# Kernel optimization log

Hardware: AMD Instinct MI355X
Metric: run time of the kernel (lower is better)

Reference implementation:

```python
import jax, jax.numpy as jnp
import numpy as np

B, T, A = 512, 64, 32
E = D = H = 512
S = 32; C = 32; SD = S * C  # stoch_dim = 1024
UNIMIX = 0.01


def _ln(x, g, b):
    m = x.mean(-1, keepdims=True)
    v = x.var(-1, keepdims=True)
    return (x - m) / jnp.sqrt(v + 1e-5) * g + b


def _mish(x):
    return x * jnp.tanh(jax.nn.softplus(x))


def _unimix_logits(raw):
    # reshape [..., S*C] -> [..., S, C], mix with uniform, back to log-space
    l = raw.reshape(raw.shape[:-1] + (S, C))
    p = jax.nn.softmax(l, axis=-1)
    p = (1.0 - UNIMIX) * p + UNIMIX / C
    return jnp.log(jnp.clip(p, 1e-8))


def setup_inputs() -> dict:
    key = jax.random.key(0)
    ks = jax.random.split(key, 16)
    n = lambda k, shape, s=0.02: (jax.random.normal(k, shape) * s).astype(jnp.float32)
    return {
        "actions": jax.random.normal(ks[0], (B, T, A), jnp.float32),
        "embeds": jax.random.normal(ks[1], (B, T, E), jnp.float32),
        # action_proj: Linear(A,H) + LayerNorm(H)
        "aw": n(ks[2], (H, A)), "ab": jnp.zeros((H,), jnp.float32),
        "ag": jnp.ones((H,), jnp.float32), "abt": jnp.zeros((H,), jnp.float32),
        # GRUCell(SD+H, D), gate order r,z,n (torch convention)
        "w_ih": n(ks[3], (3 * D, SD + H)), "w_hh": n(ks[4], (3 * D, D)),
        "b_ih": jnp.zeros((3 * D,), jnp.float32), "b_hh": jnp.zeros((3 * D,), jnp.float32),
        # prior: Linear(D,H)+LN+Mish+Linear(H,SD)
        "pr_w1": n(ks[5], (H, D)), "pr_b1": jnp.zeros((H,), jnp.float32),
        "pr_g": jnp.ones((H,), jnp.float32), "pr_bt": jnp.zeros((H,), jnp.float32),
        "pr_w2": n(ks[6], (SD, H)), "pr_b2": jnp.zeros((SD,), jnp.float32),
        # posterior: Linear(D+E,H)+LN+Mish+Linear(H,SD)
        "po_w1": n(ks[7], (H, D + E)), "po_b1": jnp.zeros((H,), jnp.float32),
        "po_g": jnp.ones((H,), jnp.float32), "po_bt": jnp.zeros((H,), jnp.float32),
        "po_w2": n(ks[8], (SD, H)), "po_b2": jnp.zeros((SD,), jnp.float32),
    }


def reference(actions, embeds, aw, ab, ag, abt, w_ih, w_hh, b_ih, b_hh,
              pr_w1, pr_b1, pr_g, pr_bt, pr_w2, pr_b2,
              po_w1, po_b1, po_g, po_bt, po_w2, po_b2):
    keys = jax.random.split(jax.random.key(42), T)

    def gru(x, h):
        gi = x @ w_ih.T + b_ih
        gh = h @ w_hh.T + b_hh
        ir, iz, inn = jnp.split(gi, 3, axis=-1)
        hr, hz, hn = jnp.split(gh, 3, axis=-1)
        r = jax.nn.sigmoid(ir + hr)
        z = jax.nn.sigmoid(iz + hz)
        n_ = jnp.tanh(inn + r * hn)
        return (1.0 - z) * n_ + z * h

    def step(carry, xs):
        deter, stoch, prev_action = carry
        embed_t, action_t, k = xs
        a = _mish(_ln(prev_action @ aw.T + ab, ag, abt))
        deter = gru(jnp.concatenate([stoch, a], axis=-1), deter)
        prior_l = _unimix_logits(
            _mish(_ln(deter @ pr_w1.T + pr_b1, pr_g, pr_bt)) @ pr_w2.T + pr_b2)
        post_l = _unimix_logits(
            _mish(_ln(jnp.concatenate([deter, embed_t], axis=-1) @ po_w1.T + po_b1,
                      po_g, po_bt)) @ po_w2.T + po_b2)
        probs = jax.nn.softmax(post_l, axis=-1)          # [B,S,C]
        idx = jax.random.categorical(k, post_l)           # [B,S]
        oh = jax.nn.one_hot(idx, C, dtype=probs.dtype)
        stoch = (oh + probs - jax.lax.stop_gradient(probs)).reshape(probs.shape[0], SD)
        state = jnp.concatenate([deter, stoch], axis=-1)  # [B, D+SD]
        return (deter, stoch, action_t), (state, prior_l, post_l)

    init = (jnp.zeros((B, D), jnp.float32),
            jnp.zeros((B, SD), jnp.float32),
            jnp.zeros((B, A), jnp.float32))
    xs = (jnp.swapaxes(embeds, 0, 1), jnp.swapaxes(actions, 0, 1), keys)
    _, (states, priors, posts) = jax.lax.scan(step, init, xs)
    return (jnp.swapaxes(states, 0, 1),   # [B,T,D+SD]
            jnp.swapaxes(priors, 0, 1),   # [B,T,S,C]
            jnp.swapaxes(posts, 0, 1))    # [B,T,S,C]
```

## Files before the change

### kernel.cpp

```cpp
#include <hip/hip_runtime.h>
#include <hip/hip_cooperative_groups.h>
#include <stdint.h>

namespace cg = cooperative_groups;

#define NT 256

struct P {
    const float *actions, *embeds, *aw, *ab, *ag, *abt;
    const float *w_ih, *w_hh, *b_ih, *b_hh;
    const float *pr_w1, *pr_b1, *pr_g, *pr_bt, *pr_w2, *pr_b2;
    const float *po_w1, *po_b1, *po_g, *po_bt, *po_w2, *po_b2;
    float *out_states, *out_priors, *out_posts;
    float *WT;
    double *deter;
    double *gh, *gi;
    double *POraw;
    double *PRraw;
    double *At0, *At1;
    int *sidx;
};


__device__ __forceinline__ double mish_d(double x) {
    double sp = fmax(x, 0.0) + log1p(exp(-fabs(x)));
    return x * tanh(sp);
}


__device__ __forceinline__ uint32_t rotl32(uint32_t v, int r) {
    return (v << r) | (v >> (32 - r));
}

__device__ __forceinline__ void tf2x32(uint32_t k0, uint32_t k1, uint32_t& x0, uint32_t& x1) {
    const uint32_t ks2 = k0 ^ k1 ^ 0x1BD11BDAu;
    const int ra[4] = {13, 15, 26, 6};
    const int rb[4] = {17, 29, 16, 24};
    x0 += k0; x1 += k1;
#pragma unroll
    for (int i = 0; i < 4; i++) { x0 += x1; x1 = rotl32(x1, ra[i]); x1 ^= x0; }
    x0 += k1; x1 += ks2 + 1u;
#pragma unroll
    for (int i = 0; i < 4; i++) { x0 += x1; x1 = rotl32(x1, rb[i]); x1 ^= x0; }
    x0 += ks2; x1 += k0 + 2u;
#pragma unroll
    for (int i = 0; i < 4; i++) { x0 += x1; x1 = rotl32(x1, ra[i]); x1 ^= x0; }
    x0 += k0; x1 += k1 + 3u;
#pragma unroll
    for (int i = 0; i < 4; i++) { x0 += x1; x1 = rotl32(x1, rb[i]); x1 ^= x0; }
    x0 += k1; x1 += ks2 + 4u;
#pragma unroll
    for (int i = 0; i < 4; i++) { x0 += x1; x1 = rotl32(x1, ra[i]); x1 ^= x0; }
    x0 += ks2; x1 += k0 + 5u;
}

__device__ __forceinline__ void step_key(int t, uint32_t& ka, uint32_t& kb) {
    uint32_t x0 = 0u, x1 = (uint32_t)t;
    tf2x32(0u, 42u, x0, x1);
    ka = x0; kb = x1;
}

__device__ __forceinline__ double gumbel_d(uint32_t n, uint32_t ka, uint32_t kb) {
    uint32_t x0 = 0u, x1 = n;
    tf2x32(ka, kb, x0, x1);
    uint32_t bits = x0 ^ x1;
    uint32_t fb = (bits >> 9) | 0x3f800000u;
    float f = __uint_as_float(fb) - 1.0f;
    double u = fmax((double)f, 1.17549435e-38);
    return -log(-log(u));
}


__device__ void act_row(const float* actions, const float* aw, const float* ab,
                        const float* ag, const float* abt, double* dst, int b, int t) {
    int l = threadIdx.x & 63;
    double x[8];
    double s = 0;
#pragma unroll
    for (int i = 0; i < 8; i++) {
        int h = l + 64 * i;
        double a = (double)ab[h];
        if (t > 0) {
            const float* ac = actions + ((long long)b * 64 + (t - 1)) * 32;
            #pragma unroll 4
            for (int k = 0; k < 32; k++)
                a += (double)ac[k] * (double)aw[h * 32 + k];
        }
        x[i] = a; s += a;
    }
#pragma unroll
    for (int m = 1; m < 64; m <<= 1) s += __shfl_xor(s, m);
    double mean = s * (1.0 / 512.0);
    double vv = 0;
#pragma unroll
    for (int i = 0; i < 8; i++) { double d = x[i] - mean; vv += d * d; }
#pragma unroll
    for (int m = 1; m < 64; m <<= 1) vv += __shfl_xor(vv, m);
    double inv = 1.0 / sqrt(vv * (1.0 / 512.0) + 1e-5);
#pragma unroll
    for (int i = 0; i < 8; i++) {
        int h = l + 64 * i;
        dst[h] = mish_d((x[i] - mean) * inv * (double)ag[h] + (double)abt[h]);
    }
}

__device__ void ln_row(double* row, const float* g, const float* bt) {
    int l = threadIdx.x & 63;
    double x[8];
    double s = 0;
#pragma unroll
    for (int i = 0; i < 8; i++) { x[i] = row[l + 64 * i]; s += x[i]; }
#pragma unroll
    for (int m = 1; m < 64; m <<= 1) s += __shfl_xor(s, m);
    double mean = s * (1.0 / 512.0);
    double vv = 0;
#pragma unroll
    for (int i = 0; i < 8; i++) { double d = x[i] - mean; vv += d * d; }
#pragma unroll
    for (int m = 1; m < 64; m <<= 1) vv += __shfl_xor(vv, m);
    double inv = 1.0 / sqrt(vv * (1.0 / 512.0) + 1e-5);
#pragma unroll
    for (int i = 0; i < 8; i++) {
        int h = l + 64 * i;
        row[h] = mish_d((x[i] - mean) * inv * (double)g[h] + (double)bt[h]);
    }
}


__device__ void tile64(const double* __restrict__ Ad, long long lda,
                       const float* __restrict__ Bp, long long ldb,
                       int m0, int n0,
                       double (&As)[2][64][17], float (&Bs)[2][64][17],
                       double (&c)[4][4]) {
    const int tid = threadIdx.x;
    const int ty = tid >> 4, tx = tid & 15;
    const int sr = tid >> 2, sk = (tid & 3) * 4;
#pragma unroll
    for (int i = 0; i < 4; i++)
#pragma unroll
        for (int j = 0; j < 4; j++) c[i][j] = 0.0;
    double ra[4]; float rb[4];
#pragma unroll
    for (int i = 0; i < 4; i++) {
        ra[i] = Ad[(long long)(m0 + sr) * lda + sk + i];
        rb[i] = Bp[(long long)(n0 + sr) * ldb + sk + i];
    }
#pragma unroll
    for (int i = 0; i < 4; i++) { As[0][sr][sk + i] = ra[i]; Bs[0][sr][sk + i] = rb[i]; }
    __syncthreads();
    int cur = 0;
    for (int kb = 0; kb < 32; kb++) {
        if (kb < 31) {
            int k0 = (kb + 1) * 16;
#pragma unroll
            for (int i = 0; i < 4; i++) {
                ra[i] = Ad[(long long)(m0 + sr) * lda + k0 + sk + i];
                rb[i] = Bp[(long long)(n0 + sr) * ldb + k0 + sk + i];
            }
        }
#pragma unroll
        for (int kk = 0; kk < 16; kk++) {
            double av[4], bv[4];
#pragma unroll
            for (int i = 0; i < 4; i++) av[i] = As[cur][ty * 4 + i][kk];
#pragma unroll
            for (int j = 0; j < 4; j++) bv[j] = (double)Bs[cur][tx * 4 + j][kk];
#pragma unroll
            for (int i = 0; i < 4; i++)
#pragma unroll
                for (int j = 0; j < 4; j++) c[i][j] = fma(av[i], bv[j], c[i][j]);
        }
        if (kb < 31) {
            int nx = cur ^ 1;
#pragma unroll
            for (int i = 0; i < 4; i++) { As[nx][sr][sk + i] = ra[i]; Bs[nx][sr][sk + i] = rb[i]; }
        }
        __syncthreads();
        cur ^= 1;
    }
}


__device__ void tile32(const double* Ad, long long ldad,
                       const float* Af, long long ldaf, int asplit,
                       const float* Bp, long long ldb, int K,
                       int m0, int n0,
                       double (&As)[2][64][17], float (&Bs)[2][64][17],
                       double* c) {
    const int tid = threadIdx.x;
    const int ty = tid >> 3, tx = tid & 7;
    const int sr = tid >> 3, sk = (tid & 7) * 2;
    double ra[2]; float rb[2];
#pragma unroll
    for (int i = 0; i < 2; i++) {
        int k = sk + i;
        ra[i] = (k < asplit) ? Ad[(long long)(m0 + sr) * ldad + k]
                             : (double)Af[(long long)(m0 + sr) * ldaf + (k - asplit)];
        rb[i] = Bp[(long long)(n0 + sr) * ldb + k];
    }
#pragma unroll
    for (int i = 0; i < 2; i++) { As[0][sr][sk + i] = ra[i]; Bs[0][sr][sk + i] = rb[i]; }
    __syncthreads();
    c[0] = c[1] = c[2] = c[3] = 0.0;
    const int nkb = K >> 4;
    int cur = 0;
    for (int kb = 0; kb < nkb; kb++) {
        if (kb + 1 < nkb) {
            int k0 = (kb + 1) << 4;
#pragma unroll
            for (int i = 0; i < 2; i++) {
                int k = k0 + sk + i;
                ra[i] = (k < asplit) ? Ad[(long long)(m0 + sr) * ldad + k]
                                     : (double)Af[(long long)(m0 + sr) * ldaf + (k - asplit)];
                rb[i] = Bp[(long long)(n0 + sr) * ldb + k];
            }
        }
#pragma unroll
        for (int kk = 0; kk < 16; kk++) {
            double a = As[cur][ty][kk];
            c[0] = fma(a, (double)Bs[cur][tx * 4 + 0][kk], c[0]);
            c[1] = fma(a, (double)Bs[cur][tx * 4 + 1][kk], c[1]);
            c[2] = fma(a, (double)Bs[cur][tx * 4 + 2][kk], c[2]);
            c[3] = fma(a, (double)Bs[cur][tx * 4 + 3][kk], c[3]);
        }
        if (kb + 1 < nkb) {
            int nx = cur ^ 1;
#pragma unroll
            for (int i = 0; i < 2; i++) { As[nx][sr][sk + i] = ra[i]; Bs[nx][sr][sk + i] = rb[i]; }
        }
        __syncthreads();
        cur ^= 1;
    }
}


__device__ void unimix_fin(const double* c, const float* bias, float* out,
                           int m0, int n0, int t) {
    const int ty = threadIdx.x >> 3, tx = threadIdx.x & 7;
    double va[4];
#pragma unroll
    for (int q = 0; q < 4; q++) va[q] = c[q] + (double)bias[n0 + tx * 4 + q];
    double mx = fmax(fmax(va[0], va[1]), fmax(va[2], va[3]));
#pragma unroll
    for (int m = 1; m < 8; m <<= 1) mx = fmax(mx, __shfl_xor(mx, m));
    double sum = 0;
#pragma unroll
    for (int q = 0; q < 4; q++) sum += exp(va[q] - mx);
#pragma unroll
    for (int m = 1; m < 8; m <<= 1) sum += __shfl_xor(sum, m);
    double rinv = 1.0 / sum;
    long long row = (long long)(m0 + ty) * 64 + t;
    float4 o;
    float* po = (float*)&o;
#pragma unroll
    for (int q = 0; q < 4; q++)
        po[q] = (float)log(0.99 * (exp(va[q] - mx) * rinv) + 0.01 / 32.0);
    *(float4*)(out + row * 1024 + n0 + tx * 4) = o;
}

__device__ void sample_fin(const double* c, const P& p, int t, int m0, int n0) {
    const int ty = threadIdx.x >> 3, tx = threadIdx.x & 7;
    int b = m0 + ty;
    double va[4];
#pragma unroll
    for (int q = 0; q < 4; q++) va[q] = c[q] + (double)p.po_b2[n0 + tx * 4 + q];
    double mx = fmax(fmax(va[0], va[1]), fmax(va[2], va[3]));
#pragma unroll
    for (int m = 1; m < 8; m <<= 1) mx = fmax(mx, __shfl_xor(mx, m));
    double sum = 0;
#pragma unroll
    for (int q = 0; q < 4; q++) sum += exp(va[q] - mx);
#pragma unroll
    for (int m = 1; m < 8; m <<= 1) sum += __shfl_xor(sum, m);
    double rinv = 1.0 / sum;
    uint32_t ka, kb;
    step_key(t, ka, kb);
    float4 o;
    float* po = (float*)&o;
    double bv = -1e300; int bc = 0;
#pragma unroll
    for (int q = 0; q < 4; q++) {
        int cc = tx * 4 + q;
        double lp = log(0.99 * (exp(va[q] - mx) * rinv) + 0.01 / 32.0);
        po[q] = (float)lp;
        double val = gumbel_d((uint32_t)(b * 1024 + n0 + cc), ka, kb) + lp;
        if (val > bv) { bv = val; bc = cc; }
    }
#pragma unroll
    for (int m = 1; m < 8; m <<= 1) {
        double ov = __shfl_xor(bv, m);
        int oc = __shfl_xor(bc, m);
        if (ov > bv || (ov == bv && oc < bc)) { bv = ov; bc = oc; }
    }
    *(float4*)(p.out_posts + ((long long)b * 64 + t) * 1024 + n0 + tx * 4) = o;
    float4 oh;
    oh.x = (tx * 4 + 0 == bc) ? 1.0f : 0.0f;
    oh.y = (tx * 4 + 1 == bc) ? 1.0f : 0.0f;
    oh.z = (tx * 4 + 2 == bc) ? 1.0f : 0.0f;
    oh.w = (tx * 4 + 3 == bc) ? 1.0f : 0.0f;
    *(float4*)(p.out_states + ((long long)b * 64 + t) * 1536 + 512 + n0 + tx * 4) = oh;
    if (tx == 0) p.sidx[b * 32 + (n0 >> 5)] = bc;
}


__global__ __launch_bounds__(NT, 2) void k_mega(P p) {
    __shared__ double As[2][64][17];
    __shared__ float  Bs[2][64][17];
    cg::grid_group grid = cg::this_grid();
    const int bid = blockIdx.x, tid = threadIdx.x;
    const int nb = gridDim.x;
    double c4[4];
    double c[4][4];

    for (int i = bid * NT + tid; i < 1024 * 1536; i += nb * NT) {
        int cc = i / 1536, n = i % 1536;
        p.WT[(long long)cc * 1536 + n] = p.w_ih[(long long)n * 1536 + cc];
    }
    for (int i = bid * NT + tid; i < 512 * 512; i += nb * NT) p.deter[i] = 0.0;
    for (int m = bid * 4 + (tid >> 6); m < 512; m += nb * 4)
        act_row(p.actions, p.aw, p.ab, p.ag, p.abt, p.At0 + (long long)m * 512, m, 0);
    grid.sync();

    for (int t = 0; t < 64; t++) {
        const double* At = (t & 1) ? p.At1 : p.At0;
        double* Atn = (t & 1) ? p.At0 : p.At1;

        for (int q = bid; q < 512; q += nb) {
            if (q < 192) {
                int tm = q / 24, tn = q % 24;
                int m0 = tm * 64, n0 = tn * 64;
                tile64(p.deter, 512, p.w_hh, 512, m0, n0, As, Bs, c);
                const int ty = tid >> 4, tx = tid & 15;
#pragma unroll
                for (int i = 0; i < 4; i++) {
                    long long mr = m0 + ty * 4 + i;
#pragma unroll
                    for (int j = 0; j < 4; j++) {
                        int n = n0 + tx * 4 + j;
                        p.gh[mr * 1536 + n] = c[i][j] + (double)p.b_hh[n];
                    }
                }
            } else if (q < 384) {
                int q2 = q - 192;
                int tm = q2 / 24, tn = q2 % 24;
                int m0 = tm * 64, n0 = tn * 64;
                tile64(At, 512, p.w_ih + 1024, 1536, m0, n0, As, Bs, c);
                const int ty = tid >> 4, tx = tid & 15;
                if (t > 0) {
                    int* sx = (int*)&As[0][0][0];
                    __syncthreads();
                    for (int i = tid; i < 64 * 32; i += NT)
                        sx[i] = p.sidx[(m0 + (i >> 5)) * 32 + (i & 31)];
                    __syncthreads();
#pragma unroll
                    for (int i = 0; i < 4; i++) {
                        int r = ty * 4 + i;
                        for (int s = 0; s < 32; s++) {
                            int cc = s * 32 + sx[r * 32 + s];
                            const float4 v = *(const float4*)(p.WT + (long long)cc * 1536 + n0 + tx * 4);
                            c[i][0] += (double)v.x; c[i][1] += (double)v.y;
                            c[i][2] += (double)v.z; c[i][3] += (double)v.w;
                        }
                    }
                    __syncthreads();
                }
#pragma unroll
                for (int i = 0; i < 4; i++) {
                    long long mr = m0 + ty * 4 + i;
#pragma unroll
                    for (int j = 0; j < 4; j++) {
                        int n = n0 + tx * 4 + j;
                        p.gi[mr * 1536 + n] = c[i][j] + (double)p.b_ih[n];
                    }
                }
            } else {
                if (t < 63) {
                    int rr = (q - 384) * 4 + (tid >> 6);
                    act_row(p.actions, p.aw, p.ab, p.ag, p.abt,
                            Atn + (long long)rr * 512, rr, t + 1);
                }
            }
        }
        grid.sync();

        for (int e = bid * NT + tid; e < 512 * 512; e += nb * NT) {
            int b = e >> 9, d = e & 511;
            long long base = (long long)b * 1536;
            double ir = p.gi[base + d],          hr = p.gh[base + d];
            double iz = p.gi[base + 512 + d],    hz = p.gh[base + 512 + d];
            double in_ = p.gi[base + 1024 + d],  hn = p.gh[base + 1024 + d];
            double h = p.deter[e];
            double rr = 1.0 / (1.0 + exp(-(ir + hr)));
            double zz = 1.0 / (1.0 + exp(-(iz + hz)));
            double nn = tanh(in_ + rr * hn);
            double dn = (1.0 - zz) * nn + zz * h;
            p.deter[e] = dn;
            p.out_states[((long long)b * 64 + t) * 1536 + d] = (float)dn;
        }
        grid.sync();

        for (int q = bid; q < 512; q += nb) {
            if (q < 256) {
                int tm = q >> 4, tn = q & 15;
                tile32(p.deter, 512, p.embeds + (long long)t * 512, 32768, 512,
                       p.po_w1, 1024, 1024, tm * 32, tn * 32, As, Bs, c4);
                const int ty = tid >> 3, tx = tid & 7;
#pragma unroll
                for (int j = 0; j < 4; j++)
                    p.POraw[(long long)(tm * 32 + ty) * 512 + tn * 32 + tx * 4 + j] =
                        c4[j] + (double)p.po_b1[tn * 32 + tx * 4 + j];
            } else {
                int q2 = q - 256;
                int tm = q2 >> 4, tn = q2 & 15;
                tile32(p.deter, 512, nullptr, 0, 512, p.pr_w1, 512, 512,
                       tm * 32, tn * 32, As, Bs, c4);
                const int ty = tid >> 3, tx = tid & 7;
#pragma unroll
                for (int j = 0; j < 4; j++)
                    p.PRraw[(long long)(tm * 32 + ty) * 512 + tn * 32 + tx * 4 + j] =
                        c4[j] + (double)p.pr_b1[tn * 32 + tx * 4 + j];
            }
        }
        grid.sync();

        for (int r = bid * 4 + (tid >> 6); r < 1024; r += nb * 4) {
            if (r < 512) ln_row(p.POraw + (long long)r * 512, p.po_g, p.po_bt);
            else         ln_row(p.PRraw + (long long)(r - 512) * 512, p.pr_g, p.pr_bt);
        }
        grid.sync();

        for (int q = bid; q < 1024; q += nb) {
            if (q < 512) {
                int tm = q >> 5, s = q & 31;
                tile32(p.POraw, 512, nullptr, 0, 512, p.po_w2, 512, 512,
                       tm * 32, s * 32, As, Bs, c4);
                sample_fin(c4, p, t, tm * 32, s * 32);
            } else {
                int q2 = q - 512;
                int tm = q2 >> 5, s = q2 & 31;
                tile32(p.PRraw, 512, nullptr, 0, 512, p.pr_w2, 512, 512,
                       tm * 32, s * 32, As, Bs, c4);
                unimix_fin(c4, p.pr_b2, p.out_priors, tm * 32, s * 32, t);
            }
        }
        grid.sync();
    }
}


extern "C" void kernel_launch(void* const* d_in, const int* in_sizes, int n_in,
                              void* d_out, int out_size, void* d_ws, size_t ws_size,
                              hipStream_t stream) {
    P p;
    p.actions = (const float*)d_in[0];
    p.embeds  = (const float*)d_in[1];
    p.aw = (const float*)d_in[2];  p.ab = (const float*)d_in[3];
    p.ag = (const float*)d_in[4];  p.abt = (const float*)d_in[5];
    p.w_ih = (const float*)d_in[6]; p.w_hh = (const float*)d_in[7];
    p.b_ih = (const float*)d_in[8]; p.b_hh = (const float*)d_in[9];
    p.pr_w1 = (const float*)d_in[10]; p.pr_b1 = (const float*)d_in[11];
    p.pr_g = (const float*)d_in[12];  p.pr_bt = (const float*)d_in[13];
    p.pr_w2 = (const float*)d_in[14]; p.pr_b2 = (const float*)d_in[15];
    p.po_w1 = (const float*)d_in[16]; p.po_b1 = (const float*)d_in[17];
    p.po_g = (const float*)d_in[18];  p.po_bt = (const float*)d_in[19];
    p.po_w2 = (const float*)d_in[20]; p.po_b2 = (const float*)d_in[21];

    float* out = (float*)d_out;
    p.out_states = out;
    p.out_priors = out + (size_t)512 * 64 * 1536;
    p.out_posts  = out + (size_t)512 * 64 * 1536 + (size_t)512 * 64 * 1024;

    char* ws = (char*)d_ws;
    size_t off = 0;
    auto carve = [&](size_t bytes) -> char* {
        char* q = ws + off;
        off = (off + bytes + 255) & ~(size_t)255;
        return q;
    };
    p.sidx  = (int*)carve((size_t)512 * 32 * 4);
    p.WT    = (float*)carve((size_t)1024 * 1536 * 4);
    p.deter = (double*)carve((size_t)512 * 512 * 8);
    p.gh    = (double*)carve((size_t)512 * 1536 * 8);
    p.gi    = (double*)carve((size_t)512 * 1536 * 8);
    p.POraw = (double*)carve((size_t)512 * 512 * 8);
    p.PRraw = (double*)carve((size_t)512 * 512 * 8);
    p.At0   = (double*)carve((size_t)512 * 512 * 8);
    p.At1   = (double*)carve((size_t)512 * 512 * 8);
    if (off > ws_size) return;

    int maxb = 0;
    hipError_t oe = hipOccupancyMaxActiveBlocksPerMultiprocessor(
        &maxb, (const void*)k_mega, NT, 0);
    int nb = (oe == hipSuccess && maxb >= 2) ? 512 : 256;

    void* args[] = { (void*)&p };
    hipLaunchCooperativeKernel((const void*)k_mega, dim3(nb), dim3(NT),
                               args, 0, stream);
}
```

Baseline: 37.40 ms.

## Shrink GRU GEMM tiles to 64x32 and raise cooperative grid occupancy

Replaces the 64x64 GRU gate tiles with 64x32 tiles over a k-step of 8, which doubles the number of GEMM work items per timestep and cuts per-thread accumulator registers. Shared buffers are flattened into smaller 1D arrays, and launch bounds go from 2 to 4 blocks per CU. The cooperative grid is now sized from the occupancy query, up to 1024 blocks, so more work runs in parallel in each grid-synced phase. The costs are more K iterations with extra syncs per tile, less register reuse per FMA, and more expensive grid.sync with more blocks.

```diff
diff --git a/kernel.cpp b/kernel.cpp
--- a/kernel.cpp
+++ b/kernel.cpp
@@ -127,53 +127,52 @@
 }
 
 
-__device__ void tile64(const double* __restrict__ Ad, long long lda,
-                       const float* __restrict__ Bp, long long ldb,
-                       int m0, int n0,
-                       double (&As)[2][64][17], float (&Bs)[2][64][17],
-                       double (&c)[4][4]) {
+__device__ void tile6432(const double* __restrict__ Ad, long long lda,
+                         const float* __restrict__ Bp, long long ldb,
+                         int m0, int n0,
+                         double (&AsD)[2][640], float (&BsF)[2][640],
+                         double (&c)[2][4]) {
     const int tid = threadIdx.x;
-    const int ty = tid >> 4, tx = tid & 15;
-    const int sr = tid >> 2, sk = (tid & 3) * 4;
-#pragma unroll
-    for (int i = 0; i < 4; i++)
+    const int ty = tid >> 3, tx = tid & 7;
+    const int ar = tid >> 2, ak = (tid & 3) * 2;
+    const int br = tid >> 3, bk = tid & 7;
+#pragma unroll
+    for (int i = 0; i < 2; i++)
 #pragma unroll
         for (int j = 0; j < 4; j++) c[i][j] = 0.0;
-    double ra[4]; float rb[4];
-#pragma unroll
-    for (int i = 0; i < 4; i++) {
-        ra[i] = Ad[(long long)(m0 + sr) * lda + sk + i];
-        rb[i] = Bp[(long long)(n0 + sr) * ldb + sk + i];
-    }
-#pragma unroll
-    for (int i = 0; i < 4; i++) { As[0][sr][sk + i] = ra[i]; Bs[0][sr][sk + i] = rb[i]; }
+    double ra[2]; float rb;
+#pragma unroll
+    for (int i = 0; i < 2; i++) ra[i] = Ad[(long long)(m0 + ar) * lda + ak + i];
+    rb = Bp[(long long)(n0 + br) * ldb + bk];
+#pragma unroll
+    for (int i = 0; i < 2; i++) AsD[0][ar * 9 + ak + i] = ra[i];
+    BsF[0][br * 9 + bk] = rb;
     __syncthreads();
     int cur = 0;
-    for (int kb = 0; kb < 32; kb++) {
-        if (kb < 31) {
-            int k0 = (kb + 1) * 16;
-#pragma unroll
-            for (int i = 0; i < 4; i++) {
-                ra[i] = Ad[(long long)(m0 + sr) * lda + k0 + sk + i];
-                rb[i] = Bp[(long long)(n0 + sr) * ldb + k0 + sk + i];
-            }
-        }
-#pragma unroll
-        for (int kk = 0; kk < 16; kk++) {
-            double av[4], bv[4];
-#pragma unroll
-            for (int i = 0; i < 4; i++) av[i] = As[cur][ty * 4 + i][kk];
-#pragma unroll
-            for (int j = 0; j < 4; j++) bv[j] = (double)Bs[cur][tx * 4 + j][kk];
-#pragma unroll
-            for (int i = 0; i < 4; i++)
+    for (int kb = 0; kb < 64; kb++) {
+        if (kb < 63) {
+            int k0 = (kb + 1) * 8;
+#pragma unroll
+            for (int i = 0; i < 2; i++) ra[i] = Ad[(long long)(m0 + ar) * lda + k0 + ak + i];
+            rb = Bp[(long long)(n0 + br) * ldb + k0 + bk];
+        }
+#pragma unroll
+        for (int kk = 0; kk < 8; kk++) {
+            double av[2], bv[4];
+#pragma unroll
+            for (int i = 0; i < 2; i++) av[i] = AsD[cur][(ty * 2 + i) * 9 + kk];
+#pragma unroll
+            for (int j = 0; j < 4; j++) bv[j] = (double)BsF[cur][(tx * 4 + j) * 9 + kk];
+#pragma unroll
+            for (int i = 0; i < 2; i++)
 #pragma unroll
                 for (int j = 0; j < 4; j++) c[i][j] = fma(av[i], bv[j], c[i][j]);
         }
-        if (kb < 31) {
+        if (kb < 63) {
             int nx = cur ^ 1;
 #pragma unroll
-            for (int i = 0; i < 4; i++) { As[nx][sr][sk + i] = ra[i]; Bs[nx][sr][sk + i] = rb[i]; }
+            for (int i = 0; i < 2; i++) AsD[nx][ar * 9 + ak + i] = ra[i];
+            BsF[nx][br * 9 + bk] = rb;
         }
         __syncthreads();
         cur ^= 1;
@@ -185,7 +184,7 @@
                        const float* Af, long long ldaf, int asplit,
                        const float* Bp, long long ldb, int K,
                        int m0, int n0,
-                       double (&As)[2][64][17], float (&Bs)[2][64][17],
+                       double (&AsD)[2][640], float (&BsF)[2][640],
                        double* c) {
     const int tid = threadIdx.x;
     const int ty = tid >> 3, tx = tid & 7;
@@ -199,7 +198,7 @@
         rb[i] = Bp[(long long)(n0 + sr) * ldb + k];
     }
 #pragma unroll
-    for (int i = 0; i < 2; i++) { As[0][sr][sk + i] = ra[i]; Bs[0][sr][sk + i] = rb[i]; }
+    for (int i = 0; i < 2; i++) { AsD[0][sr * 17 + sk + i] = ra[i]; BsF[0][sr * 17 + sk + i] = rb[i]; }
     __syncthreads();
     c[0] = c[1] = c[2] = c[3] = 0.0;
     const int nkb = K >> 4;
@@ -217,16 +216,16 @@
         }
 #pragma unroll
         for (int kk = 0; kk < 16; kk++) {
-            double a = As[cur][ty][kk];
-            c[0] = fma(a, (double)Bs[cur][tx * 4 + 0][kk], c[0]);
-            c[1] = fma(a, (double)Bs[cur][tx * 4 + 1][kk], c[1]);
-            c[2] = fma(a, (double)Bs[cur][tx * 4 + 2][kk], c[2]);
-            c[3] = fma(a, (double)Bs[cur][tx * 4 + 3][kk], c[3]);
+            double a = AsD[cur][ty * 17 + kk];
+            c[0] = fma(a, (double)BsF[cur][(tx * 4 + 0) * 17 + kk], c[0]);
+            c[1] = fma(a, (double)BsF[cur][(tx * 4 + 1) * 17 + kk], c[1]);
+            c[2] = fma(a, (double)BsF[cur][(tx * 4 + 2) * 17 + kk], c[2]);
+            c[3] = fma(a, (double)BsF[cur][(tx * 4 + 3) * 17 + kk], c[3]);
         }
         if (kb + 1 < nkb) {
             int nx = cur ^ 1;
 #pragma unroll
-            for (int i = 0; i < 2; i++) { As[nx][sr][sk + i] = ra[i]; Bs[nx][sr][sk + i] = rb[i]; }
+            for (int i = 0; i < 2; i++) { AsD[nx][sr * 17 + sk + i] = ra[i]; BsF[nx][sr * 17 + sk + i] = rb[i]; }
         }
         __syncthreads();
         cur ^= 1;
@@ -303,14 +302,14 @@
 }
 
 
-__global__ __launch_bounds__(NT, 2) void k_mega(P p) {
-    __shared__ double As[2][64][17];
-    __shared__ float  Bs[2][64][17];
+__global__ __launch_bounds__(NT, 4) void k_mega(P p) {
+    __shared__ double AsD[2][640];
+    __shared__ float  BsF[2][640];
     cg::grid_group grid = cg::this_grid();
     const int bid = blockIdx.x, tid = threadIdx.x;
     const int nb = gridDim.x;
     double c4[4];
-    double c[4][4];
+    double c[2][4];
 
     for (int i = bid * NT + tid; i < 1024 * 1536; i += nb * NT) {
         int cc = i / 1536, n = i % 1536;
@@ -325,36 +324,36 @@
         const double* At = (t & 1) ? p.At1 : p.At0;
         double* Atn = (t & 1) ? p.At0 : p.At1;
 
-        for (int q = bid; q < 512; q += nb) {
-            if (q < 192) {
-                int tm = q / 24, tn = q % 24;
-                int m0 = tm * 64, n0 = tn * 64;
-                tile64(p.deter, 512, p.w_hh, 512, m0, n0, As, Bs, c);
-                const int ty = tid >> 4, tx = tid & 15;
-#pragma unroll
-                for (int i = 0; i < 4; i++) {
-                    long long mr = m0 + ty * 4 + i;
+        for (int q = bid; q < 896; q += nb) {
+            if (q < 384) {
+                int tm = q / 48, tn = q % 48;
+                int m0 = tm * 64, n0 = tn * 32;
+                tile6432(p.deter, 512, p.w_hh, 512, m0, n0, AsD, BsF, c);
+                const int ty = tid >> 3, tx = tid & 7;
+#pragma unroll
+                for (int i = 0; i < 2; i++) {
+                    long long mr = m0 + ty * 2 + i;
 #pragma unroll
                     for (int j = 0; j < 4; j++) {
                         int n = n0 + tx * 4 + j;
                         p.gh[mr * 1536 + n] = c[i][j] + (double)p.b_hh[n];
                     }
                 }
-            } else if (q < 384) {
-                int q2 = q - 192;
-                int tm = q2 / 24, tn = q2 % 24;
-                int m0 = tm * 64, n0 = tn * 64;
-                tile64(At, 512, p.w_ih + 1024, 1536, m0, n0, As, Bs, c);
-                const int ty = tid >> 4, tx = tid & 15;
+            } else if (q < 768) {
+                int q2 = q - 384;
+                int tm = q2 / 48, tn = q2 % 48;
+                int m0 = tm * 64, n0 = tn * 32;
+                tile6432(At, 512, p.w_ih + 1024, 1536, m0, n0, AsD, BsF, c);
+                const int ty = tid >> 3, tx = tid & 7;
                 if (t > 0) {
-                    int* sx = (int*)&As[0][0][0];
+                    int* sx = (int*)&AsD[0][0];
                     __syncthreads();
                     for (int i = tid; i < 64 * 32; i += NT)
                         sx[i] = p.sidx[(m0 + (i >> 5)) * 32 + (i & 31)];
                     __syncthreads();
 #pragma unroll
-                    for (int i = 0; i < 4; i++) {
-                        int r = ty * 4 + i;
+                    for (int i = 0; i < 2; i++) {
+                        int r = ty * 2 + i;
                         for (int s = 0; s < 32; s++) {
                             int cc = s * 32 + sx[r * 32 + s];
                             const float4 v = *(const float4*)(p.WT + (long long)cc * 1536 + n0 + tx * 4);
@@ -365,8 +364,8 @@
                     __syncthreads();
                 }
 #pragma unroll
-                for (int i = 0; i < 4; i++) {
-                    long long mr = m0 + ty * 4 + i;
+                for (int i = 0; i < 2; i++) {
+                    long long mr = m0 + ty * 2 + i;
 #pragma unroll
                     for (int j = 0; j < 4; j++) {
                         int n = n0 + tx * 4 + j;
@@ -375,7 +374,7 @@
                 }
             } else {
                 if (t < 63) {
-                    int rr = (q - 384) * 4 + (tid >> 6);
+                    int rr = (q - 768) * 4 + (tid >> 6);
                     act_row(p.actions, p.aw, p.ab, p.ag, p.abt,
                             Atn + (long long)rr * 512, rr, t + 1);
                 }
@@ -403,7 +402,7 @@
             if (q < 256) {
                 int tm = q >> 4, tn = q & 15;
                 tile32(p.deter, 512, p.embeds + (long long)t * 512, 32768, 512,
-                       p.po_w1, 1024, 1024, tm * 32, tn * 32, As, Bs, c4);
+                       p.po_w1, 1024, 1024, tm * 32, tn * 32, AsD, BsF, c4);
                 const int ty = tid >> 3, tx = tid & 7;
 #pragma unroll
                 for (int j = 0; j < 4; j++)
@@ -413,7 +412,7 @@
                 int q2 = q - 256;
                 int tm = q2 >> 4, tn = q2 & 15;
                 tile32(p.deter, 512, nullptr, 0, 512, p.pr_w1, 512, 512,
-                       tm * 32, tn * 32, As, Bs, c4);
+                       tm * 32, tn * 32, AsD, BsF, c4);
                 const int ty = tid >> 3, tx = tid & 7;
 #pragma unroll
                 for (int j = 0; j < 4; j++)
@@ -433,13 +432,13 @@
             if (q < 512) {
                 int tm = q >> 5, s = q & 31;
                 tile32(p.POraw, 512, nullptr, 0, 512, p.po_w2, 512, 512,
-                       tm * 32, s * 32, As, Bs, c4);
+                       tm * 32, s * 32, AsD, BsF, c4);
                 sample_fin(c4, p, t, tm * 32, s * 32);
             } else {
                 int q2 = q - 512;
                 int tm = q2 >> 5, s = q2 & 31;
                 tile32(p.PRraw, 512, nullptr, 0, 512, p.pr_w2, 512, 512,
-                       tm * 32, s * 32, As, Bs, c4);
+                       tm * 32, s * 32, AsD, BsF, c4);
                 unimix_fin(c4, p.pr_b2, p.out_priors, tm * 32, s * 32, t);
             }
         }
@@ -491,7 +490,9 @@
     int maxb = 0;
     hipError_t oe = hipOccupancyMaxActiveBlocksPerMultiprocessor(
         &maxb, (const void*)k_mega, NT, 0);
-    int nb = (oe == hipSuccess && maxb >= 2) ? 512 : 256;
+    if (oe != hipSuccess || maxb < 1) maxb = 1;
+    if (maxb > 4) maxb = 4;
+    int nb = 256 * maxb;
 
     void* args[] = { (void*)&p };
     hipLaunchCooperativeKernel((const void*)k_mega, dim3(nb), dim3(NT),
```

Measured after the change: 35.15 ms. 6.0% less time.
